# Kernel tuning notes

Measured on AMD Instinct MI355X. Metric: run time of the kernel, lower is better.

## Reference

```python
import jax, jax.numpy as jnp
import numpy as np

N_NODES = 27
SRC = jnp.array([0,1,1,1,1,2,2,2,3,3,3,4,4,4,5,5,5,5,6,6,6,6,6,7,7,7,8,8,8,9,9,9,10,10,10,11,11,11,12,12,12,13,13,13,14,14,14,15,15,15,16,16,16,17,17,17,18,18,18,18,19,20,21,21,21,22,23,23,23,24,25,26], dtype=jnp.int32)
DST = jnp.array([1,0,2,4,6,1,3,7,2,4,24,1,3,5,4,6,17,19,1,5,7,8,10,2,6,23,6,9,16,8,10,13,6,9,11,10,12,23,11,13,21,9,12,14,13,15,20,14,16,18,8,15,17,5,16,18,15,17,25,26,5,14,12,22,23,21,7,11,21,3,18,18], dtype=jnp.int32)


def _conv2d(x, w, b):
    # x: [BN, Cin, H, W], w: [Cout, Cin, 3, 3] -> SAME padding conv
    y = jax.lax.conv_general_dilated(x, w, window_strides=(1, 1), padding='SAME',
                                     dimension_numbers=('NCHW', 'OIHW', 'NCHW'))
    return y + b[None, :, None, None]


def _block(h, w, b):
    # h: [B, N, Cin, H, W]; Conv2dMessage (conv -> scatter-add over edges) + LeakyReLU(0.2) + MaxPool2d(2)
    B, N, C, H, W = h.shape
    y = _conv2d(h.reshape(B * N, C, H, W), w, b).reshape(B, N, -1, H, W)
    # propagate with aggr='add': out[dst] += y[src]; isolated-in nodes become zero
    agg = jnp.zeros_like(y).at[:, DST].add(y[:, SRC])
    a = jax.nn.leaky_relu(agg, negative_slope=0.2)
    Co = a.shape[2]
    p = jax.lax.reduce_window(a.reshape(B * N, Co, H, W), -jnp.inf, jax.lax.max,
                              (1, 1, 2, 2), (1, 1, 2, 2), 'VALID')
    return p.reshape(B, N, Co, H // 2, W // 2)


def setup_inputs() -> dict:
    key = jax.random.key(0)
    ks = jax.random.split(key, 9)
    B, Cin, H, W = 32, 4, 64, 64
    x = jax.random.normal(ks[0], (B, Cin, H, W), dtype=jnp.float32)
    def kaiming(k, shape):
        fan_in = int(np.prod(shape[1:]))
        bound = float(np.sqrt(6.0 / fan_in))
        return jax.random.uniform(k, shape, jnp.float32, -bound, bound)
    w1 = kaiming(ks[1], (32, Cin, 3, 3)); b1 = jnp.zeros((32,), jnp.float32)
    w2 = kaiming(ks[2], (64, 32, 3, 3));  b2 = jnp.zeros((64,), jnp.float32)
    w3 = kaiming(ks[3], (128, 64, 3, 3)); b3 = jnp.zeros((128,), jnp.float32)
    wc = kaiming(ks[4], (1, 128));        bc = jnp.zeros((1,), jnp.float32)
    return {"x": x, "w1": w1, "b1": b1, "w2": w2, "b2": b2,
            "w3": w3, "b3": b3, "wc": wc, "bc": bc}


def reference(x, w1, b1, w2, b2, w3, b3, wc, bc):
    B = x.shape[0]
    # torch.tile(xi, (27,1,1,1)) vectorized over batch -> [B, 27, C, H, W]
    h = jnp.broadcast_to(x[:, None], (B, N_NODES) + x.shape[1:])
    h = _block(h, w1, b1)   # [B, 27, 32, 32, 32]
    h = _block(h, w2, b2)   # [B, 27, 64, 16, 16]
    h = _block(h, w3, b3)   # [B, 27, 128, 8, 8]
    feat = h.mean(axis=(3, 4))                 # AdaptiveAvgPool2d(1) + flatten -> [B, 27, 128]
    logits = jnp.einsum('bnc,oc->bno', feat, wc) + bc  # [B, 27, 1]
    return logits[:, 0, :]                     # classifier(xi)[0] per sample -> [B, 1]
```

## Files before the change

kernel.cpp:

```cpp
#include <hip/hip_runtime.h>


#define LRELU(v) fmaxf((v), 0.2f * (v))

#define P1H_ELEMS (32 * 32 * 34 * 36)
#define P2H_ELEMS (32 * 64 * 18 * 20)

__global__ __launch_bounds__(256, 4) void k1(const float* __restrict__ x,
                                             const float* __restrict__ w1,
                                             const float* __restrict__ b1,
                                             float* __restrict__ P1H) {
    __shared__ __align__(16) float obuf[1152];
    const int bx = blockIdx.x;
    const int b  = blockIdx.y;
    const int rb = bx & 3, cog = bx >> 2;
    const int t  = threadIdx.x;
    const int l  = t & 63, wv = t >> 6;
    const int r  = l >> 4, q = l & 15;
    const int row0 = 16 * rb + 4 * wv + r;

    for (int i = t; i < 288; i += 256)
        *(float4*)&obuf[4 * i] = make_float4(0.f, 0.f, 0.f, 0.f);
    __syncthreads();

    const bool cL = (q > 0), cR = (q < 15);
    bool rv[3];
    #pragma unroll
    for (int d = 0; d < 3; ++d) rv[d] = (unsigned)(row0 - 1 + d) < 64u;

    float acc[4][4];
    #pragma unroll
    for (int g = 0; g < 4; ++g) {
        float bias = b1[cog * 4 + g];
        acc[g][0] = bias; acc[g][1] = bias; acc[g][2] = bias; acc[g][3] = bias;
    }

    #pragma unroll
    for (int c = 0; c < 4; ++c) {
        float win[3][6];
        #pragma unroll
        for (int d = 0; d < 3; ++d) {
            int base = ((b * 4 + c) * 64 + (row0 - 1 + d)) * 64;
            int iL = base + 4 * q - 2;
            int i4 = base + 4 * q;
            int iR = base + 4 * q + 4;
            iL = max(iL, 0); iL = min(iL, 32 * 4 * 64 * 64 - 2);
            i4 = max(i4, 0); i4 = min(i4, 32 * 4 * 64 * 64 - 4);
            iR = max(iR, 0); iR = min(iR, 32 * 4 * 64 * 64 - 2);
            float2 L  = *(const float2*)(x + iL);
            float4 M  = *(const float4*)(x + i4);
            float2 R2 = *(const float2*)(x + iR);
            win[d][0] = (rv[d] && cL) ? L.y : 0.f;
            win[d][1] = rv[d] ? M.x : 0.f;
            win[d][2] = rv[d] ? M.y : 0.f;
            win[d][3] = rv[d] ? M.z : 0.f;
            win[d][4] = rv[d] ? M.w : 0.f;
            win[d][5] = (rv[d] && cR) ? R2.x : 0.f;
        }
        #pragma unroll
        for (int g = 0; g < 4; ++g) {
            const float* wp = &w1[((cog * 4 + g) * 4 + c) * 9];
            #pragma unroll
            for (int d = 0; d < 3; ++d)
                #pragma unroll
                for (int j = 0; j < 3; ++j) {
                    float w = wp[3 * d + j];
                    acc[g][0] += w * win[d][j];
                    acc[g][1] += w * win[d][j + 1];
                    acc[g][2] += w * win[d][j + 2];
                    acc[g][3] += w * win[d][j + 3];
                }
        }
    }

    const int prow_l = 2 * wv + (r >> 1);
    #pragma unroll
    for (int g = 0; g < 4; ++g) {
        float m0 = fmaxf(LRELU(acc[g][0]), LRELU(acc[g][1]));
        float m1 = fmaxf(LRELU(acc[g][2]), LRELU(acc[g][3]));
        float p0 = fmaxf(m0, __shfl_xor(m0, 16));
        float p1 = fmaxf(m1, __shfl_xor(m1, 16));
        if ((r & 1) == 0) {
            obuf[(g * 8 + prow_l) * 36 + 2 * q + 1] = 12.f * p0;
            obuf[(g * 8 + prow_l) * 36 + 2 * q + 2] = 12.f * p1;
        }
    }
    __syncthreads();

    for (int i = t; i < 288; i += 256) {
        int co_l = i / 72, rem = i % 72, pr = rem / 9, cw = rem % 9;
        *(float4*)&P1H[((b * 32 + cog * 4 + co_l) * 34 + 8 * rb + pr + 1) * 36 + 4 * cw] =
            *(const float4*)&obuf[4 * i];
    }
    if (rb == 0 || rb == 3) {
        int h = rb ? 33 : 0;
        for (int i = t; i < 36; i += 256) {
            int co_l = i / 9, cw = i % 9;
            *(float4*)&P1H[((b * 32 + cog * 4 + co_l) * 34 + h) * 36 + 4 * cw] =
                make_float4(0.f, 0.f, 0.f, 0.f);
        }
    }
}

__global__ __launch_bounds__(256, 2) void k2(const float* __restrict__ P1H,
                                             const float* __restrict__ w2,
                                             const float* __restrict__ b2,
                                             float* __restrict__ p2H) {
    __shared__ __align__(16) float wtile[12288];
    __shared__ __align__(16) float xin[1728];
    __shared__ __align__(16) float obuf[1280];
    const int bx = blockIdx.x;
    const int b  = blockIdx.y;
    const int cog = bx >> 3, rs = bx & 7;
    const int t  = threadIdx.x, l = t & 63;
    const int wvs = __builtin_amdgcn_readfirstlane(t >> 6);
    const int q  = l & 15, R = l >> 4;

    for (int i = t; i < 2304; i += 256) {
        float4 v = *(const float4*)&w2[cog * 9216 + 4 * i];
        int e = 4 * i;
        wtile[((e + 0) / 9) * 12 + (e + 0) % 9] = v.x;
        wtile[((e + 1) / 9) * 12 + (e + 1) % 9] = v.y;
        wtile[((e + 2) / 9) * 12 + (e + 2) % 9] = v.z;
        wtile[((e + 3) / 9) * 12 + (e + 3) % 9] = v.w;
    }
    for (int i = t; i < 320; i += 256)
        *(float4*)&obuf[4 * i] = make_float4(0.f, 0.f, 0.f, 0.f);

    float acc[8][2];
    #pragma unroll
    for (int g = 0; g < 8; ++g) {
        float bias = 4.f * b2[cog * 32 + wvs * 8 + g];
        acc[g][0] = bias; acc[g][1] = bias;
    }

    for (int cc = 0; cc < 4; ++cc) {
        __syncthreads();
        for (int i = t; i < 432; i += 256) {
            int cin_l = i / 54, rem = i % 54;
            *(float4*)&xin[cin_l * 216 + 4 * rem] =
                *(const float4*)&P1H[((b * 32 + cc * 8 + cin_l) * 34 + rs * 4) * 36 + 4 * rem];
        }
        __syncthreads();
        #pragma unroll
        for (int cl = 0; cl < 8; ++cl) {
            float win[3][4];
            #pragma unroll
            for (int d = 0; d < 3; ++d) {
                const float* xr = &xin[cl * 216 + (R + d) * 36 + 2 * q];
                float2 a = *(const float2*)xr;
                float2 c = *(const float2*)(xr + 2);
                win[d][0] = a.x; win[d][1] = a.y; win[d][2] = c.x; win[d][3] = c.y;
            }
            const int cin = cc * 8 + cl;
            #pragma unroll
            for (int g = 0; g < 8; ++g) {
                const float* wg = &wtile[((wvs * 8 + g) * 32 + cin) * 12];
                float4 wa = *(const float4*)wg;
                float4 wb = *(const float4*)(wg + 4);
                float  w8 = wg[8];
                float wt[9] = {wa.x, wa.y, wa.z, wa.w, wb.x, wb.y, wb.z, wb.w, w8};
                #pragma unroll
                for (int d = 0; d < 3; ++d)
                    #pragma unroll
                    for (int j = 0; j < 3; ++j) {
                        float w = wt[3 * d + j];
                        acc[g][0] += w * win[d][j];
                        acc[g][1] += w * win[d][j + 1];
                    }
            }
        }
    }

    #pragma unroll
    for (int g = 0; g < 8; ++g) {
        float m = fmaxf(LRELU(acc[g][0]), LRELU(acc[g][1]));
        float p = fmaxf(m, __shfl_xor(m, 16));
        if ((R & 1) == 0)
            obuf[((wvs * 8 + g) * 2 + (R >> 1)) * 20 + q + 1] = p;
    }
    __syncthreads();

    for (int i = t; i < 320; i += 256) {
        int co_l = i / 10, rem = i % 10, pr = rem / 5, cw = rem % 5;
        *(float4*)&p2H[((b * 64 + cog * 32 + co_l) * 18 + rs * 2 + pr + 1) * 20 + 4 * cw] =
            *(const float4*)&obuf[4 * i];
    }
    if (rs == 0 || rs == 7) {
        int h2 = rs ? 17 : 0;
        for (int i = t; i < 160; i += 256) {
            int co_l = i / 5, cw = i % 5;
            *(float4*)&p2H[((b * 64 + cog * 32 + co_l) * 18 + h2) * 20 + 4 * cw] =
                make_float4(0.f, 0.f, 0.f, 0.f);
        }
    }
}

__global__ __launch_bounds__(256, 2) void k3(const float* __restrict__ p2H,
                                             const float* __restrict__ w3,
                                             const float* __restrict__ b3,
                                             const float* __restrict__ wc,
                                             const float* __restrict__ bc,
                                             float* __restrict__ out) {
    __shared__ __align__(16) float smem[6912];
    const int cog = blockIdx.x;
    const int b   = blockIdx.y;
    const int c0  = cog * 8;
    const int t   = threadIdx.x, l = t & 63;
    const int wvs = __builtin_amdgcn_readfirstlane(t >> 6);
    const int r   = l >> 2, q = l & 3;

    for (int i = t; i < 1152; i += 256) {
        float4 v = *(const float4*)&w3[cog * 4608 + 4 * i];
        int e = 4 * i;
        smem[((e + 0) / 9) * 12 + (e + 0) % 9] = v.x;
        smem[((e + 1) / 9) * 12 + (e + 1) % 9] = v.y;
        smem[((e + 2) / 9) * 12 + (e + 2) % 9] = v.z;
        smem[((e + 3) / 9) * 12 + (e + 3) % 9] = v.w;
    }
    __syncthreads();

    float acc[8][4];
    #pragma unroll
    for (int g = 0; g < 8; ++g) {
        float bias = (wvs == 0) ? b3[c0 + g] : 0.f;
        acc[g][0] = bias; acc[g][1] = bias; acc[g][2] = bias; acc[g][3] = bias;
    }

    #pragma unroll 4
    for (int cl = 0; cl < 16; ++cl) {
        const int cin = wvs * 16 + cl;
        const float* pb = p2H + (((b * 64 + cin) * 18 + r) * 20 + 4 * q);
        float win[3][6];
        #pragma unroll
        for (int d = 0; d < 3; ++d) {
            float4 M  = *(const float4*)(pb + d * 20);
            float2 Rt = *(const float2*)(pb + d * 20 + 4);
            win[d][0] = M.x; win[d][1] = M.y; win[d][2] = M.z;
            win[d][3] = M.w; win[d][4] = Rt.x; win[d][5] = Rt.y;
        }
        #pragma unroll
        for (int g = 0; g < 8; ++g) {
            const float* wg = &smem[(g * 64 + cin) * 12];
            float4 wa = *(const float4*)wg;
            float4 wb = *(const float4*)(wg + 4);
            float  w8 = wg[8];
            float wt[9] = {wa.x, wa.y, wa.z, wa.w, wb.x, wb.y, wb.z, wb.w, w8};
            #pragma unroll
            for (int d = 0; d < 3; ++d)
                #pragma unroll
                for (int j = 0; j < 3; ++j) {
                    float w = wt[3 * d + j];
                    acc[g][0] += w * win[d][j];
                    acc[g][1] += w * win[d][j + 1];
                    acc[g][2] += w * win[d][j + 2];
                    acc[g][3] += w * win[d][j + 3];
                }
        }
    }

    __syncthreads();
    if (wvs > 0) {
        float* cb = &smem[((wvs - 1) * 64 + l) * 36];
        #pragma unroll
        for (int g = 0; g < 8; ++g)
            *(float4*)&cb[g * 4] =
                make_float4(acc[g][0], acc[g][1], acc[g][2], acc[g][3]);
    }
    __syncthreads();

    if (wvs == 0) {
        #pragma unroll
        for (int k = 0; k < 3; ++k) {
            const float* cb = &smem[(k * 64 + l) * 36];
            #pragma unroll
            for (int g = 0; g < 8; ++g) {
                float4 v = *(const float4*)&cb[g * 4];
                acc[g][0] += v.x; acc[g][1] += v.y;
                acc[g][2] += v.z; acc[g][3] += v.w;
            }
        }
        float vsum = 0.f;
        #pragma unroll
        for (int g = 0; g < 8; ++g) {
            float m0 = fmaxf(LRELU(acc[g][0]), LRELU(acc[g][1]));
            float m1 = fmaxf(LRELU(acc[g][2]), LRELU(acc[g][3]));
            float pm0 = fmaxf(m0, __shfl_xor(m0, 4));
            float pm1 = fmaxf(m1, __shfl_xor(m1, 4));
            float contrib = ((r & 1) == 0) ? (pm0 + pm1) : 0.f;
            vsum += contrib * wc[c0 + g];
        }
        #pragma unroll
        for (int off = 32; off > 0; off >>= 1) vsum += __shfl_xor(vsum, off);
        if (l == 0) {
            float o = vsum * (1.f / 64.f);
            if (cog == 0) o += bc[0];
            atomicAdd(&out[b], o);
        }
    }
}

extern "C" void kernel_launch(void* const* d_in, const int* in_sizes, int n_in,
                              void* d_out, int out_size, void* d_ws, size_t ws_size,
                              hipStream_t stream) {
    const float* x  = (const float*)d_in[0];
    const float* w1 = (const float*)d_in[1];
    const float* b1 = (const float*)d_in[2];
    const float* w2 = (const float*)d_in[3];
    const float* b2 = (const float*)d_in[4];
    const float* w3 = (const float*)d_in[5];
    const float* b3 = (const float*)d_in[6];
    const float* wc = (const float*)d_in[7];
    const float* bc = (const float*)d_in[8];
    float* out = (float*)d_out;

    float* P1H = (float*)d_ws;
    float* p2H = P1H + P1H_ELEMS;

    hipMemsetAsync(out, 0, 32 * sizeof(float), stream);
    k1<<<dim3(32, 32), 256, 0, stream>>>(x, w1, b1, P1H);
    k2<<<dim3(16, 32), 256, 0, stream>>>(P1H, w2, b2, p2H);
    k3<<<dim3(16, 32), 256, 0, stream>>>(p2H, w3, b3, wc, bc, out);
}
```

Before: 140.4 us.

## Halve k2 output channels per block, raise occupancy, fold output memset into k1

```diff
diff --git a/kernel.cpp b/kernel.cpp
--- a/kernel.cpp
+++ b/kernel.cpp
@@ -9,7 +9,8 @@
 __global__ __launch_bounds__(256, 4) void k1(const float* __restrict__ x,
                                              const float* __restrict__ w1,
                                              const float* __restrict__ b1,
-                                             float* __restrict__ P1H) {
+                                             float* __restrict__ P1H,
+                                             float* __restrict__ out) {
     __shared__ __align__(16) float obuf[1152];
     const int bx = blockIdx.x;
     const int b  = blockIdx.y;
@@ -19,14 +20,15 @@
     const int r  = l >> 4, q = l & 15;
     const int row0 = 16 * rb + 4 * wv + r;
 
+    if (bx == 0 && t == 0) out[b] = 0.f;
+
     for (int i = t; i < 288; i += 256)
         *(float4*)&obuf[4 * i] = make_float4(0.f, 0.f, 0.f, 0.f);
     __syncthreads();
 
     const bool cL = (q > 0), cR = (q < 15);
-    bool rv[3];
-    #pragma unroll
-    for (int d = 0; d < 3; ++d) rv[d] = (unsigned)(row0 - 1 + d) < 64u;
+    const int colL = max(4 * q - 2, 0);
+    const int colR = min(4 * q + 4, 62);
 
     float acc[4][4];
     #pragma unroll
@@ -40,22 +42,19 @@
         float win[3][6];
         #pragma unroll
         for (int d = 0; d < 3; ++d) {
-            int base = ((b * 4 + c) * 64 + (row0 - 1 + d)) * 64;
-            int iL = base + 4 * q - 2;
-            int i4 = base + 4 * q;
-            int iR = base + 4 * q + 4;
-            iL = max(iL, 0); iL = min(iL, 32 * 4 * 64 * 64 - 2);
-            i4 = max(i4, 0); i4 = min(i4, 32 * 4 * 64 * 64 - 4);
-            iR = max(iR, 0); iR = min(iR, 32 * 4 * 64 * 64 - 2);
-            float2 L  = *(const float2*)(x + iL);
-            float4 M  = *(const float4*)(x + i4);
-            float2 R2 = *(const float2*)(x + iR);
-            win[d][0] = (rv[d] && cL) ? L.y : 0.f;
-            win[d][1] = rv[d] ? M.x : 0.f;
-            win[d][2] = rv[d] ? M.y : 0.f;
-            win[d][3] = rv[d] ? M.z : 0.f;
-            win[d][4] = rv[d] ? M.w : 0.f;
-            win[d][5] = (rv[d] && cR) ? R2.x : 0.f;
+            int gr = row0 - 1 + d;
+            bool v = (unsigned)gr < 64u;
+            int grc = min(max(gr, 0), 63);
+            const float* row = x + ((b * 4 + c) * 64 + grc) * 64;
+            float2 L  = *(const float2*)(row + colL);
+            float4 M  = *(const float4*)(row + 4 * q);
+            float2 R2 = *(const float2*)(row + colR);
+            win[d][0] = (v && cL) ? L.y : 0.f;
+            win[d][1] = v ? M.x : 0.f;
+            win[d][2] = v ? M.y : 0.f;
+            win[d][3] = v ? M.z : 0.f;
+            win[d][4] = v ? M.w : 0.f;
+            win[d][5] = (v && cR) ? R2.x : 0.f;
         }
         #pragma unroll
         for (int g = 0; g < 4; ++g) {
@@ -102,35 +101,36 @@
     }
 }
 
-__global__ __launch_bounds__(256, 2) void k2(const float* __restrict__ P1H,
+__global__ __launch_bounds__(256, 4) void k2(const float* __restrict__ P1H,
                                              const float* __restrict__ w2,
                                              const float* __restrict__ b2,
                                              float* __restrict__ p2H) {
-    __shared__ __align__(16) float wtile[12288];
+    __shared__ __align__(16) float wtile[6144];
     __shared__ __align__(16) float xin[1728];
-    __shared__ __align__(16) float obuf[1280];
+    __shared__ __align__(16) float obuf[640];
     const int bx = blockIdx.x;
     const int b  = blockIdx.y;
     const int cog = bx >> 3, rs = bx & 7;
+    const int c0  = cog * 16;
     const int t  = threadIdx.x, l = t & 63;
     const int wvs = __builtin_amdgcn_readfirstlane(t >> 6);
     const int q  = l & 15, R = l >> 4;
 
-    for (int i = t; i < 2304; i += 256) {
-        float4 v = *(const float4*)&w2[cog * 9216 + 4 * i];
+    for (int i = t; i < 1152; i += 256) {
+        float4 v = *(const float4*)&w2[cog * 4608 + 4 * i];
         int e = 4 * i;
         wtile[((e + 0) / 9) * 12 + (e + 0) % 9] = v.x;
         wtile[((e + 1) / 9) * 12 + (e + 1) % 9] = v.y;
         wtile[((e + 2) / 9) * 12 + (e + 2) % 9] = v.z;
         wtile[((e + 3) / 9) * 12 + (e + 3) % 9] = v.w;
     }
-    for (int i = t; i < 320; i += 256)
+    for (int i = t; i < 160; i += 256)
         *(float4*)&obuf[4 * i] = make_float4(0.f, 0.f, 0.f, 0.f);
 
-    float acc[8][2];
-    #pragma unroll
-    for (int g = 0; g < 8; ++g) {
-        float bias = 4.f * b2[cog * 32 + wvs * 8 + g];
+    float acc[4][2];
+    #pragma unroll
+    for (int g = 0; g < 4; ++g) {
+        float bias = 4.f * b2[c0 + wvs * 4 + g];
         acc[g][0] = bias; acc[g][1] = bias;
     }
 
@@ -154,8 +154,8 @@
             }
             const int cin = cc * 8 + cl;
             #pragma unroll
-            for (int g = 0; g < 8; ++g) {
-                const float* wg = &wtile[((wvs * 8 + g) * 32 + cin) * 12];
+            for (int g = 0; g < 4; ++g) {
+                const float* wg = &wtile[((wvs * 4 + g) * 32 + cin) * 12];
                 float4 wa = *(const float4*)wg;
                 float4 wb = *(const float4*)(wg + 4);
                 float  w8 = wg[8];
@@ -173,30 +173,30 @@
     }
 
     #pragma unroll
-    for (int g = 0; g < 8; ++g) {
+    for (int g = 0; g < 4; ++g) {
         float m = fmaxf(LRELU(acc[g][0]), LRELU(acc[g][1]));
         float p = fmaxf(m, __shfl_xor(m, 16));
         if ((R & 1) == 0)
-            obuf[((wvs * 8 + g) * 2 + (R >> 1)) * 20 + q + 1] = p;
-    }
-    __syncthreads();
-
-    for (int i = t; i < 320; i += 256) {
+            obuf[((wvs * 4 + g) * 2 + (R >> 1)) * 20 + q + 1] = p;
+    }
+    __syncthreads();
+
+    for (int i = t; i < 160; i += 256) {
         int co_l = i / 10, rem = i % 10, pr = rem / 5, cw = rem % 5;
-        *(float4*)&p2H[((b * 64 + cog * 32 + co_l) * 18 + rs * 2 + pr + 1) * 20 + 4 * cw] =
+        *(float4*)&p2H[((b * 64 + c0 + co_l) * 18 + rs * 2 + pr + 1) * 20 + 4 * cw] =
             *(const float4*)&obuf[4 * i];
     }
     if (rs == 0 || rs == 7) {
         int h2 = rs ? 17 : 0;
-        for (int i = t; i < 160; i += 256) {
+        for (int i = t; i < 80; i += 256) {
             int co_l = i / 5, cw = i % 5;
-            *(float4*)&p2H[((b * 64 + cog * 32 + co_l) * 18 + h2) * 20 + 4 * cw] =
+            *(float4*)&p2H[((b * 64 + c0 + co_l) * 18 + h2) * 20 + 4 * cw] =
                 make_float4(0.f, 0.f, 0.f, 0.f);
         }
     }
 }
 
-__global__ __launch_bounds__(256, 2) void k3(const float* __restrict__ p2H,
+__global__ __launch_bounds__(256, 4) void k3(const float* __restrict__ p2H,
                                              const float* __restrict__ w3,
                                              const float* __restrict__ b3,
                                              const float* __restrict__ wc,
@@ -317,8 +317,7 @@
     float* P1H = (float*)d_ws;
     float* p2H = P1H + P1H_ELEMS;
 
-    hipMemsetAsync(out, 0, 32 * sizeof(float), stream);
-    k1<<<dim3(32, 32), 256, 0, stream>>>(x, w1, b1, P1H);
-    k2<<<dim3(16, 32), 256, 0, stream>>>(P1H, w2, b2, p2H);
+    k1<<<dim3(32, 32), 256, 0, stream>>>(x, w1, b1, P1H, out);
+    k2<<<dim3(32, 32), 256, 0, stream>>>(P1H, w2, b2, p2H);
     k3<<<dim3(16, 32), 256, 0, stream>>>(p2H, w3, b3, wc, bc, out);
 }
```

New measurement: 139.8 us. Within noise of the previous version (-0.4%).
